# Kernel optimization log

Measured on AMD Instinct MI355X. Metric: run time of the kernel, lower is better.

## Reference

```python
import jax, jax.numpy as jnp
import numpy as np

B, S, E, H = 2, 2048, 1024, 16
D = E // H  # head dimension = 64


def setup_inputs() -> dict:
    key = jax.random.key(0)
    ks = jax.random.split(key, 12)
    scale_in = 1.0 / np.sqrt(E)
    x = jax.random.normal(ks[0], (B, S, E), dtype=jnp.float32)
    # random 0/1 attention mask (1 = attend, 0 = masked out)
    mask = jax.random.randint(ks[1], (B, S, S), 0, 2, dtype=jnp.int32)
    # per-head QKV projections, stacked over the head axis: [H, E, D]
    Wq = jax.random.normal(ks[2], (H, E, D), dtype=jnp.float32) * scale_in
    bq = jnp.zeros((H, D), dtype=jnp.float32)
    Wk = jax.random.normal(ks[3], (H, E, D), dtype=jnp.float32) * scale_in
    bk = jnp.zeros((H, D), dtype=jnp.float32)
    Wv = jax.random.normal(ks[4], (H, E, D), dtype=jnp.float32) * scale_in
    bv = jnp.zeros((H, D), dtype=jnp.float32)
    # output projection: [H*D, E] == [E, E]
    Wo = jax.random.normal(ks[5], (H * D, E), dtype=jnp.float32) * scale_in
    bo = jnp.zeros((E,), dtype=jnp.float32)
    return {"x": x, "mask": mask, "Wq": Wq, "bq": bq, "Wk": Wk, "bk": bk,
            "Wv": Wv, "bv": bv, "Wo": Wo, "bo": bo}


def reference(x, mask, Wq, bq, Wk, bk, Wv, bv, Wo, bo):
    # Batched equivalent of the per-head Python loop: all heads at once.
    q = jnp.einsum('bse,hed->bhsd', x, Wq) + bq[None, :, None, :]  # [B,H,S,D]
    k = jnp.einsum('bse,hed->bhsd', x, Wk) + bk[None, :, None, :]
    v = jnp.einsum('bse,hed->bhsd', x, Wv) + bv[None, :, None, :]
    scale = 1.0 / jnp.sqrt(jnp.asarray(D, dtype=q.dtype))
    scores = jnp.einsum('bhsd,bhtd->bhst', q, k) * scale          # [B,H,S,S]
    scores = jnp.where(mask[:, None, :, :] != 0, scores, jnp.asarray(-1e9, scores.dtype))
    attn = jax.nn.softmax(scores, axis=-1)
    ctx = jnp.einsum('bhst,bhtd->bhsd', attn, v)                  # [B,H,S,D]
    # concat heads along feature dim (torch.cat(dim=2))
    concat = jnp.transpose(ctx, (0, 2, 1, 3)).reshape(B, S, H * D)
    return concat @ Wo + bo
```

## Files before the change

kernel.cpp:

```cpp
#include <hip/hip_runtime.h>

#define S_LEN 2048
#define EMB   1024
#define NH    16
#define HD    64
#define BS    2

typedef __bf16 bf16;
typedef bf16  bf16x8 __attribute__((ext_vector_type(8)));
typedef bf16  bf16x4 __attribute__((ext_vector_type(4)));
typedef float f32x4  __attribute__((ext_vector_type(4)));
typedef unsigned long long u64;

__device__ __forceinline__ bf16x8 ld8(const bf16* p){ return *(const bf16x8*)p; }

#define SW(row, g) ((((g) ^ ((row) & 7))) * 8)

__global__ __launch_bounds__(256)
void pack_mask(const int* __restrict__ mask, u64* __restrict__ pm)
{
    int lane = threadIdx.x & 63;
    int row  = blockIdx.x * 4 + (threadIdx.x >> 6);
    const int* mr = mask + (size_t)row * S_LEN;
    u64* pr = pm + (size_t)row * (S_LEN / 64);
    for (int i = 0; i < S_LEN / 64; ++i) {
        u64 bits = __ballot(mr[i * 64 + lane] != 0);
        if (lane == 0) pr[i] = bits;
    }
}

__global__ __launch_bounds__(256)
void transpose_w(const float* __restrict__ W0, const float* __restrict__ W1,
                 const float* __restrict__ W2, const float* __restrict__ W3,
                 bf16* __restrict__ Wt)
{
    const int z = blockIdx.z;
    const float* W = z == 0 ? W0 : z == 1 ? W1 : z == 2 ? W2 : W3;
    const bool head = z < 3;
    const int k0 = blockIdx.x * 64, n0 = blockIdx.y * 64;
    const int tid = threadIdx.x;
    __shared__ float T[64][68];
    {
        int k = k0 + (tid >> 2), cg = (tid & 3) * 16;
        size_t base = head ? ((size_t)(n0 >> 6) * ((size_t)EMB * HD) + (size_t)k * HD + cg)
                           : ((size_t)k * EMB + n0 + cg);
        #pragma unroll
        for (int g = 0; g < 4; ++g) {
            f32x4 v = *(const f32x4*)(W + base + g * 4);
            #pragma unroll
            for (int j = 0; j < 4; ++j) T[tid >> 2][cg + g * 4 + j] = v[j];
        }
    }
    __syncthreads();
    {
        int n = n0 + (tid >> 2), ck = (tid & 3) * 16;
        bf16 t16[16];
        #pragma unroll
        for (int j = 0; j < 16; ++j) t16[j] = (bf16)T[ck + j][tid >> 2];
        bf16* outp = Wt + (size_t)z * EMB * EMB + (size_t)n * EMB + k0 + ck;
        *(bf16x8*)outp       = *(bf16x8*)t16;
        *(bf16x8*)(outp + 8) = *(bf16x8*)(t16 + 8);
    }
}

__global__ __launch_bounds__(256)
void cvt_f32_bf16(const float* __restrict__ x, bf16* __restrict__ y)
{
    size_t i = ((size_t)blockIdx.x * 256 + threadIdx.x) * 16;
    bf16 t[16];
    #pragma unroll
    for (int g = 0; g < 4; ++g) {
        f32x4 v = *(const f32x4*)(x + i + g * 4);
        #pragma unroll
        for (int j = 0; j < 4; ++j) t[g * 4 + j] = (bf16)v[j];
    }
    *(bf16x8*)(y + i)     = *(bf16x8*)t;
    *(bf16x8*)(y + i + 8) = *(bf16x8*)(t + 8);
}

__global__ __launch_bounds__(512)
void gemm128(const void* __restrict__ Ap, const float* __restrict__ Wp,
             const bf16* __restrict__ Wtp, const float* __restrict__ bias,
             void* __restrict__ Cp, int N, int K, int whead,
             int m_base, int a32, int cmode)
{
    const int tid  = threadIdx.x;
    const int lane = tid & 63, quad = lane >> 4, c = lane & 15;
    const int w = tid >> 6, wm = w >> 2, wn = w & 3;
    const int m0 = blockIdx.x * 128, n0 = blockIdx.y * 128;

    __shared__ bf16 Ash[128][64];
    __shared__ bf16 Wsh[128][64];

    f32x4 acc[4][2];
    #pragma unroll
    for (int mt = 0; mt < 4; ++mt)
        #pragma unroll
        for (int nt = 0; nt < 2; ++nt) acc[mt][nt] = (f32x4){0.f,0.f,0.f,0.f};

    const int arow = tid >> 2, aq = tid & 3;

    auto compute = [&]() {
        #pragma unroll
        for (int kh = 0; kh < 2; ++kh) {
            bf16x8 bfr[2];
            #pragma unroll
            for (int nt = 0; nt < 2; ++nt) {
                int rw = wn * 32 + nt * 16 + c;
                bfr[nt] = ld8(&Wsh[rw][SW(rw, kh * 4 + quad)]);
            }
            #pragma unroll
            for (int mt = 0; mt < 4; ++mt) {
                int ra = wm * 64 + mt * 16 + c;
                bf16x8 af = ld8(&Ash[ra][SW(ra, kh * 4 + quad)]);
                #pragma unroll
                for (int nt = 0; nt < 2; ++nt)
                    acc[mt][nt] = __builtin_amdgcn_mfma_f32_16x16x32_bf16(af, bfr[nt], acc[mt][nt], 0, 0, 0);
            }
        }
    };

    if (Wtp) {
        bf16x8 ar[2]; f32x4 a32r[4]; bf16x8 wr[2];
        auto loadT = [&](int k0) {
            if (a32) {
                const float* A = (const float*)Ap + (size_t)(m_base + m0 + arow) * K + k0 + aq * 16;
                #pragma unroll
                for (int g = 0; g < 4; ++g) a32r[g] = *(const f32x4*)(A + g * 4);
            } else {
                const bf16* A = (const bf16*)Ap + (size_t)(m_base + m0 + arow) * K + k0 + aq * 16;
                ar[0] = ld8(A); ar[1] = ld8(A + 8);
            }
            const bf16* Wr = Wtp + (size_t)(n0 + arow) * K + k0 + aq * 16;
            wr[0] = ld8(Wr); wr[1] = ld8(Wr + 8);
        };
        auto storeT = [&]() {
            bf16x8 av[2];
            if (a32) {
                bf16 t16[16];
                #pragma unroll
                for (int g = 0; g < 4; ++g)
                    #pragma unroll
                    for (int j = 0; j < 4; ++j) t16[g * 4 + j] = (bf16)a32r[g][j];
                av[0] = *(bf16x8*)t16; av[1] = *(bf16x8*)(t16 + 8);
            } else { av[0] = ar[0]; av[1] = ar[1]; }
            #pragma unroll
            for (int g2 = 0; g2 < 2; ++g2) {
                *(bf16x8*)&Ash[arow][SW(arow, aq * 2 + g2)] = av[g2];
                *(bf16x8*)&Wsh[arow][SW(arow, aq * 2 + g2)] = wr[g2];
            }
        };
        loadT(0);
        for (int k0 = 0; k0 < K; k0 += 64) {
            __syncthreads();
            storeT();
            __syncthreads();
            if (k0 + 64 < K) loadT(k0 + 64);
            compute();
        }
    } else {
        for (int k0 = 0; k0 < K; k0 += 64) {
            __syncthreads();
            if (a32) {
                const float* A = (const float*)Ap + (size_t)(m_base + m0 + arow) * K + k0 + aq * 16;
                bf16 t16[16];
                #pragma unroll
                for (int g = 0; g < 4; ++g) {
                    f32x4 v = *(const f32x4*)(A + g * 4);
                    #pragma unroll
                    for (int j = 0; j < 4; ++j) t16[g * 4 + j] = (bf16)v[j];
                }
                *(bf16x8*)&Ash[arow][SW(arow, aq * 2)]     = *(bf16x8*)t16;
                *(bf16x8*)&Ash[arow][SW(arow, aq * 2 + 1)] = *(bf16x8*)(t16 + 8);
            } else {
                const bf16* A = (const bf16*)Ap + (size_t)(m_base + m0 + arow) * K + k0 + aq * 16;
                *(bf16x8*)&Ash[arow][SW(arow, aq * 2)]     = ld8(A);
                *(bf16x8*)&Ash[arow][SW(arow, aq * 2 + 1)] = ld8(A + 8);
            }
            {
                int nl = tid & 127, kg = tid >> 7;
                int n = n0 + nl;
                size_t base    = whead ? ((size_t)(n >> 6) * ((size_t)K * HD) + (n & 63))
                                       : (size_t)n;
                size_t kstride = whead ? (size_t)HD : (size_t)N;
                #pragma unroll
                for (int p = 0; p < 2; ++p) {
                    int grp = kg + 4 * p;
                    bf16 t8[8];
                    #pragma unroll
                    for (int j = 0; j < 8; ++j)
                        t8[j] = (bf16)Wp[base + (size_t)(k0 + grp * 8 + j) * kstride];
                    *(bf16x8*)&Wsh[nl][SW(nl, grp)] = *(bf16x8*)t8;
                }
            }
            __syncthreads();
            compute();
        }
    }

    #pragma unroll
    for (int nt = 0; nt < 2; ++nt) {
        int n = n0 + wn * 32 + nt * 16 + c;
        float bv = bias[n];
        #pragma unroll
        for (int mt = 0; mt < 4; ++mt)
            #pragma unroll
            for (int r = 0; r < 4; ++r) {
                int m = m0 + wm * 64 + mt * 16 + quad * 4 + r;
                float v = acc[mt][nt][r] + bv;
                if (cmode == 0)      ((bf16*)Cp)[(size_t)m * N + n] = (bf16)v;
                else if (cmode == 1) ((float*)Cp)[(size_t)m * N + n] = v;
                else {
                    int mm = m_base + m;
                    ((bf16*)Cp)[((size_t)((mm >> 11) * NH + (n >> 6)) * HD + (n & 63)) * S_LEN + (mm & 2047)] = (bf16)v;
                }
            }
    }
}

__global__ __launch_bounds__(256)
void attn_kernel(bf16* q0p, bf16* q1p, const bf16* __restrict__ kbuf,
                 const bf16* __restrict__ VTg, const u64* __restrict__ pmask)
{
    const int tid  = threadIdx.x;
    const int w    = tid >> 6;
    const int lane = tid & 63;
    const int quad = lane >> 4;
    const int c    = lane & 15;
    const int q0   = blockIdx.x * 128;
    const int bh   = blockIdx.y;
    const int b    = bh >> 4, h = bh & 15;

    bf16* qc = b ? q1p : q0p;
    const bf16* kh_ = kbuf + (size_t)b * S_LEN * EMB + h * HD;
    const bf16* vt  = VTg + (size_t)bh * HD * S_LEN;

    __shared__ bf16 Ksh [64][64];
    __shared__ bf16 VTsh[64][64];
    __shared__ bf16 Psh[4][32][64];

    bf16x8 qf[2][2];
    #pragma unroll
    for (int st = 0; st < 2; ++st)
        #pragma unroll
        for (int kk = 0; kk < 2; ++kk)
            qf[st][kk] = ld8(qc + (size_t)(q0 + w * 32 + st * 16 + c) * EMB + h * HD + kk * 32 + quad * 8);

    const u64* pmr0 = pmask + (size_t)(b * S_LEN + q0 + w * 32 + c) * (S_LEN / 64);
    const u64* pmr1 = pmr0 + (size_t)16 * (S_LEN / 64);

    float l[2] = {0.f, 0.f};
    f32x4 o[2][4];
    #pragma unroll
    for (int st = 0; st < 2; ++st)
        #pragma unroll
        for (int dt = 0; dt < 4; ++dt) o[st][dt] = (f32x4){0.f,0.f,0.f,0.f};

    const int srow = tid >> 2, sg = (tid & 3) * 2;
    bf16x8 kr[2], vr[2];
    auto loadKV = [&](int t0) {
        const bf16* kp = kh_ + (size_t)(t0 + srow) * EMB + sg * 8;
        kr[0] = ld8(kp); kr[1] = ld8(kp + 8);
        const bf16* vp = vt + (size_t)srow * S_LEN + t0 + sg * 8;
        vr[0] = ld8(vp); vr[1] = ld8(vp + 8);
    };

    loadKV(0);
    for (int t0 = 0; t0 < S_LEN; t0 += 64) {
        __syncthreads();
        #pragma unroll
        for (int g2 = 0; g2 < 2; ++g2) {
            *(bf16x8*)&Ksh [srow][SW(srow, sg + g2)] = kr[g2];
            *(bf16x8*)&VTsh[srow][SW(srow, sg + g2)] = vr[g2];
        }
        __syncthreads();
        if (t0 + 64 < S_LEN) loadKV(t0 + 64);

        u64 pm0 = pmr0[t0 >> 6], pm1 = pmr1[t0 >> 6];

        f32x4 sc[2][4];
        #pragma unroll
        for (int st = 0; st < 2; ++st)
            #pragma unroll
            for (int tt = 0; tt < 4; ++tt) sc[st][tt] = (f32x4){0.f,0.f,0.f,0.f};
        #pragma unroll
        for (int tt = 0; tt < 4; ++tt)
            #pragma unroll
            for (int kk = 0; kk < 2; ++kk) {
                int rk = tt * 16 + c;
                bf16x8 ka = ld8(&Ksh[rk][SW(rk, kk * 4 + quad)]);
                sc[0][tt] = __builtin_amdgcn_mfma_f32_16x16x32_bf16(ka, qf[0][kk], sc[0][tt], 0, 0, 0);
                sc[1][tt] = __builtin_amdgcn_mfma_f32_16x16x32_bf16(ka, qf[1][kk], sc[1][tt], 0, 0, 0);
            }

        #pragma unroll
        for (int st = 0; st < 2; ++st) {
            u64 pm = st ? pm1 : pm0;
            int prow = st * 16 + c;
            #pragma unroll
            for (int tt = 0; tt < 4; ++tt) {
                bf16x4 pv;
                #pragma unroll
                for (int r = 0; r < 4; ++r) {
                    float e = __expf(sc[st][tt][r] * 0.125f);
                    e = ((pm >> (tt * 16 + quad * 4 + r)) & 1) ? e : 0.f;
                    l[st] += e;
                    pv[r] = (bf16)e;
                }
                *(bf16x4*)&Psh[w][prow][SW(prow, tt * 2 + (quad >> 1)) + (quad & 1) * 4] = pv;
            }
        }
        __builtin_amdgcn_s_waitcnt(0xc07f);

        #pragma unroll
        for (int th = 0; th < 2; ++th) {
            bf16x8 pf0 = ld8(&Psh[w][c]     [SW(c,      th * 4 + quad)]);
            bf16x8 pf1 = ld8(&Psh[w][16 + c][SW(16 + c, th * 4 + quad)]);
            #pragma unroll
            for (int dt = 0; dt < 4; ++dt) {
                int rv = dt * 16 + c;
                bf16x8 av = ld8(&VTsh[rv][SW(rv, th * 4 + quad)]);
                o[0][dt] = __builtin_amdgcn_mfma_f32_16x16x32_bf16(av, pf0, o[0][dt], 0, 0, 0);
                o[1][dt] = __builtin_amdgcn_mfma_f32_16x16x32_bf16(av, pf1, o[1][dt], 0, 0, 0);
            }
        }
    }

    #pragma unroll
    for (int st = 0; st < 2; ++st) {
        float ls = l[st];
        ls += __shfl_xor(ls, 16);
        ls += __shfl_xor(ls, 32);
        float inv = 1.0f / fmaxf(ls, 1e-30f);
        #pragma unroll
        for (int dt = 0; dt < 4; ++dt) {
            bf16x4 ov;
            #pragma unroll
            for (int r = 0; r < 4; ++r) ov[r] = (bf16)(o[st][dt][r] * inv);
            *(bf16x4*)&qc[(size_t)(q0 + w * 32 + st * 16 + c) * EMB + h * HD + dt * 16 + quad * 4] = ov;
        }
    }
}

extern "C" void kernel_launch(void* const* d_in, const int* in_sizes, int n_in,
                              void* d_out, int out_size, void* d_ws, size_t ws_size,
                              hipStream_t stream)
{
    const float* x    = (const float*)d_in[0];
    const int*   mask = (const int*)d_in[1];
    const float* Wq   = (const float*)d_in[2];
    const float* bq   = (const float*)d_in[3];
    const float* Wk   = (const float*)d_in[4];
    const float* bk   = (const float*)d_in[5];
    const float* Wv   = (const float*)d_in[6];
    const float* bv   = (const float*)d_in[7];
    const float* Wo   = (const float*)d_in[8];
    const float* bo   = (const float*)d_in[9];
    float* out = (float*)d_out;

    const size_t SLAB = (size_t)S_LEN * EMB;
    const size_t QB = (size_t)BS * SLAB * sizeof(bf16);
    const size_t WT = (size_t)4 * EMB * EMB * sizeof(bf16);
    const size_t PM = (size_t)BS * S_LEN * (S_LEN / 64) * 8;
    const size_t XB = (size_t)BS * SLAB * sizeof(bf16);

    bf16* VT = (bf16*)d_out;
    bf16* kb = (bf16*)d_out + BS * SLAB;

    dim3 b256(256), b512(512);
    dim3 gFull(BS * S_LEN / 128, EMB / 128);
    dim3 gHalf(S_LEN / 128, EMB / 128);
    dim3 gAtt (S_LEN / 128, BS * NH);
    dim3 gT   (EMB / 64, EMB / 64, 4);
    dim3 gPk  (BS * S_LEN / 4);

    if (ws_size >= QB + WT + PM + 64) {
        bf16* qb  = (bf16*)d_ws;
        bf16* Wt  = (bf16*)((char*)d_ws + QB);
        u64*  pm  = (u64*)((char*)d_ws + QB + WT);
        const void* xA = x; int a32 = 1;
        if (ws_size >= QB + WT + PM + XB + 64) {
            bf16* xbf = (bf16*)((char*)d_ws + QB + WT + PM);
            cvt_f32_bf16<<<dim3(1024), b256, 0, stream>>>(x, xbf);
            xA = xbf; a32 = 0;
        }
        pack_mask<<<gPk, b256, 0, stream>>>(mask, pm);
        transpose_w<<<gT, b256, 0, stream>>>(Wq, Wk, Wv, Wo, Wt);

        gemm128<<<gFull, b512, 0, stream>>>(xA, nullptr, Wt + 1 * EMB * EMB, bk, kb, EMB, EMB, 0, 0, a32, 0);
        gemm128<<<gFull, b512, 0, stream>>>(xA, nullptr, Wt + 2 * EMB * EMB, bv, VT, EMB, EMB, 0, 0, a32, 2);
        gemm128<<<gFull, b512, 0, stream>>>(xA, nullptr, Wt + 0 * EMB * EMB, bq, qb, EMB, EMB, 0, 0, a32, 0);

        attn_kernel<<<gAtt, b256, 0, stream>>>(qb, qb + SLAB, kb, VT, pm);

        gemm128<<<gFull, b512, 0, stream>>>(qb, nullptr, Wt + 3 * EMB * EMB, bo, out, EMB, EMB, 0, 0, 0, 1);
    } else if (ws_size >= QB + PM + 64) {
        bf16* qb = (bf16*)d_ws;
        u64*  pm = (u64*)((char*)d_ws + QB);
        pack_mask<<<gPk, b256, 0, stream>>>(mask, pm);

        gemm128<<<gFull, b512, 0, stream>>>(x, Wk, nullptr, bk, kb, EMB, EMB, 1, 0, 1, 0);
        gemm128<<<gFull, b512, 0, stream>>>(x, Wv, nullptr, bv, VT, EMB, EMB, 1, 0, 1, 2);
        gemm128<<<gFull, b512, 0, stream>>>(x, Wq, nullptr, bq, qb, EMB, EMB, 1, 0, 1, 0);

        attn_kernel<<<gAtt, b256, 0, stream>>>(qb, qb + SLAB, kb, VT, pm);

        gemm128<<<gFull, b512, 0, stream>>>(qb, Wo, nullptr, bo, out, EMB, EMB, 0, 0, 0, 1);
    } else {
        bf16* qb0 = (bf16*)d_in[4];
        bf16* qb1 = (bf16*)d_in[6];
        u64*  pm  = (u64*)d_in[2];

        gemm128<<<gFull, b512, 0, stream>>>(x, Wk, nullptr, bk, kb, EMB, EMB, 1, 0, 1, 0);
        gemm128<<<gFull, b512, 0, stream>>>(x, Wv, nullptr, bv, VT, EMB, EMB, 1, 0, 1, 2);
        gemm128<<<gHalf, b512, 0, stream>>>(x, Wq, nullptr, bq, qb0, EMB, EMB, 1, 0,     1, 0);
        gemm128<<<gHalf, b512, 0, stream>>>(x, Wq, nullptr, bq, qb1, EMB, EMB, 1, S_LEN, 1, 0);
        pack_mask<<<gPk, b256, 0, stream>>>(mask, pm);

        attn_kernel<<<gAtt, b256, 0, stream>>>(qb0, qb1, kb, VT, pm);

        gemm128<<<gHalf, b512, 0, stream>>>(qb0, Wo, nullptr, bo, out,        EMB, EMB, 0, 0, 0, 1);
        gemm128<<<gHalf, b512, 0, stream>>>(qb1, Wo, nullptr, bo, out + SLAB, EMB, EMB, 0, 0, 0, 1);
    }
}
```

Before: 288.5 us.

## Fuse QKV GEMMs, use direct global-to-LDS loads, fold softmax scale into Q

```diff
diff --git a/kernel.cpp b/kernel.cpp
--- a/kernel.cpp
+++ b/kernel.cpp
@@ -5,14 +5,23 @@
 #define NH    16
 #define HD    64
 #define BS    2
+#define QSCALE 0.18033688f
 
 typedef __bf16 bf16;
 typedef bf16  bf16x8 __attribute__((ext_vector_type(8)));
 typedef bf16  bf16x4 __attribute__((ext_vector_type(4)));
 typedef float f32x4  __attribute__((ext_vector_type(4)));
 typedef unsigned long long u64;
+typedef unsigned int u32;
 
 __device__ __forceinline__ bf16x8 ld8(const bf16* p){ return *(const bf16x8*)p; }
+
+__device__ __forceinline__ void gl_lds16(const bf16* g, void* l) {
+    __builtin_amdgcn_global_load_lds(
+        (const __attribute__((address_space(1))) void*)g,
+        (__attribute__((address_space(3))) void*)l,
+        16, 0, 0);
+}
 
 #define SW(row, g) ((((g) ^ ((row) & 7))) * 8)
 
@@ -78,6 +87,166 @@
     *(bf16x8*)(y + i + 8) = *(bf16x8*)(t + 8);
 }
 
+__global__ __launch_bounds__(256)
+void scale_q(bf16* __restrict__ q)
+{
+    size_t i = ((size_t)blockIdx.x * 256 + threadIdx.x) * 8;
+    bf16x8 v = *(bf16x8*)(q + i);
+    #pragma unroll
+    for (int j = 0; j < 8; ++j) v[j] = (bf16)((float)v[j] * QSCALE);
+    *(bf16x8*)(q + i) = v;
+}
+
+__global__ __launch_bounds__(256)
+void gemm_qkv(const void* __restrict__ Ap, const bf16* __restrict__ Wt,
+              const float* __restrict__ bqp, const float* __restrict__ bkp,
+              const float* __restrict__ bvp,
+              bf16* __restrict__ qb, bf16* __restrict__ kb, bf16* __restrict__ VT,
+              int a32)
+{
+    const int tid  = threadIdx.x;
+    const int lane = tid & 63, quad = lane >> 4, c = lane & 15;
+    const int w = tid >> 6, wm = w >> 1, wn = w & 1;
+    const int m0 = blockIdx.x * 128;
+    const int n0 = blockIdx.y * 128;
+
+    __shared__ bf16 Ash[128][64];
+    __shared__ bf16 Wsh[128][64];
+
+    f32x4 acc[4][4];
+    #pragma unroll
+    for (int mt = 0; mt < 4; ++mt)
+        #pragma unroll
+        for (int nt = 0; nt < 4; ++nt) acc[mt][nt] = (f32x4){0.f,0.f,0.f,0.f};
+
+    const int lrow = lane >> 3, lcol = (lane & 7) * 8;
+
+    for (int k0 = 0; k0 < EMB; k0 += 64) {
+        __syncthreads();
+        if (!a32) {
+            const bf16* A = (const bf16*)Ap;
+            #pragma unroll
+            for (int j = 0; j < 4; ++j)
+                gl_lds16(A + (size_t)(m0 + w * 32 + j * 8 + lrow) * EMB + k0 + lcol,
+                         &Ash[w * 32 + j * 8][0]);
+        } else {
+            const float* A = (const float*)Ap + (size_t)(m0 + (tid >> 1)) * EMB + k0 + (tid & 1) * 32;
+            bf16 t[32];
+            #pragma unroll
+            for (int g = 0; g < 8; ++g) {
+                f32x4 v = *(const f32x4*)(A + g * 4);
+                #pragma unroll
+                for (int j = 0; j < 4; ++j) t[g * 4 + j] = (bf16)v[j];
+            }
+            #pragma unroll
+            for (int g2 = 0; g2 < 4; ++g2)
+                *(bf16x8*)&Ash[tid >> 1][(tid & 1) * 32 + g2 * 8] = *(bf16x8*)(t + g2 * 8);
+        }
+        #pragma unroll
+        for (int j = 0; j < 4; ++j)
+            gl_lds16(Wt + (size_t)(n0 + w * 32 + j * 8 + lrow) * EMB + k0 + lcol,
+                     &Wsh[w * 32 + j * 8][0]);
+        __syncthreads();
+
+        #pragma unroll
+        for (int kh = 0; kh < 2; ++kh) {
+            bf16x8 af[4], bfv[4];
+            #pragma unroll
+            for (int mt = 0; mt < 4; ++mt) af[mt]  = ld8(&Ash[wm * 64 + mt * 16 + c][kh * 32 + quad * 8]);
+            #pragma unroll
+            for (int nt = 0; nt < 4; ++nt) bfv[nt] = ld8(&Wsh[wn * 64 + nt * 16 + c][kh * 32 + quad * 8]);
+            #pragma unroll
+            for (int mt = 0; mt < 4; ++mt)
+                #pragma unroll
+                for (int nt = 0; nt < 4; ++nt)
+                    acc[mt][nt] = __builtin_amdgcn_mfma_f32_16x16x32_bf16(af[mt], bfv[nt], acc[mt][nt], 0, 0, 0);
+        }
+    }
+
+    const int z = n0 >> 10;
+    const float* bias = z == 0 ? bqp : z == 1 ? bkp : bvp;
+    #pragma unroll
+    for (int nt = 0; nt < 4; ++nt) {
+        int nn = (n0 & 1023) + wn * 64 + nt * 16 + c;
+        float bv_ = bias[nn];
+        #pragma unroll
+        for (int mt = 0; mt < 4; ++mt)
+            #pragma unroll
+            for (int r = 0; r < 4; ++r) {
+                int m = m0 + wm * 64 + mt * 16 + quad * 4 + r;
+                float v = acc[mt][nt][r] + bv_;
+                if (z == 0)      qb[(size_t)m * EMB + nn] = (bf16)(v * QSCALE);
+                else if (z == 1) kb[(size_t)m * EMB + nn] = (bf16)v;
+                else {
+                    int head = nn >> 6, d = nn & 63;
+                    VT[((size_t)((m >> 11) * NH + head) * HD + d) * S_LEN + (m & 2047)] = (bf16)v;
+                }
+            }
+    }
+}
+
+__global__ __launch_bounds__(256)
+void gemm_o(const bf16* __restrict__ Ap, const bf16* __restrict__ Wt,
+            const float* __restrict__ bo, float* __restrict__ C)
+{
+    const int tid  = threadIdx.x;
+    const int lane = tid & 63, quad = lane >> 4, c = lane & 15;
+    const int w = tid >> 6, wm = w >> 1, wn = w & 1;
+    const int m0 = blockIdx.x * 128;
+    const int n0 = blockIdx.y * 64;
+
+    __shared__ bf16 Ash[128][64];
+    __shared__ bf16 Wsh[64][64];
+
+    f32x4 acc[4][2];
+    #pragma unroll
+    for (int mt = 0; mt < 4; ++mt)
+        #pragma unroll
+        for (int nt = 0; nt < 2; ++nt) acc[mt][nt] = (f32x4){0.f,0.f,0.f,0.f};
+
+    const int lrow = lane >> 3, lcol = (lane & 7) * 8;
+
+    for (int k0 = 0; k0 < EMB; k0 += 64) {
+        __syncthreads();
+        #pragma unroll
+        for (int j = 0; j < 4; ++j)
+            gl_lds16(Ap + (size_t)(m0 + w * 32 + j * 8 + lrow) * EMB + k0 + lcol,
+                     &Ash[w * 32 + j * 8][0]);
+        #pragma unroll
+        for (int j = 0; j < 2; ++j)
+            gl_lds16(Wt + (size_t)(n0 + w * 16 + j * 8 + lrow) * EMB + k0 + lcol,
+                     &Wsh[w * 16 + j * 8][0]);
+        __syncthreads();
+
+        #pragma unroll
+        for (int kh = 0; kh < 2; ++kh) {
+            bf16x8 af[4], bfv[2];
+            #pragma unroll
+            for (int mt = 0; mt < 4; ++mt) af[mt]  = ld8(&Ash[wm * 64 + mt * 16 + c][kh * 32 + quad * 8]);
+            #pragma unroll
+            for (int nt = 0; nt < 2; ++nt) bfv[nt] = ld8(&Wsh[wn * 32 + nt * 16 + c][kh * 32 + quad * 8]);
+            #pragma unroll
+            for (int mt = 0; mt < 4; ++mt)
+                #pragma unroll
+                for (int nt = 0; nt < 2; ++nt)
+                    acc[mt][nt] = __builtin_amdgcn_mfma_f32_16x16x32_bf16(af[mt], bfv[nt], acc[mt][nt], 0, 0, 0);
+        }
+    }
+
+    #pragma unroll
+    for (int nt = 0; nt < 2; ++nt) {
+        int n = n0 + wn * 32 + nt * 16 + c;
+        float bv_ = bo[n];
+        #pragma unroll
+        for (int mt = 0; mt < 4; ++mt)
+            #pragma unroll
+            for (int r = 0; r < 4; ++r) {
+                int m = m0 + wm * 64 + mt * 16 + quad * 4 + r;
+                C[(size_t)m * EMB + n] = acc[mt][nt][r] + bv_;
+            }
+    }
+}
+
 __global__ __launch_bounds__(512)
 void gemm128(const void* __restrict__ Ap, const float* __restrict__ Wp,
              const bf16* __restrict__ Wtp, const float* __restrict__ bias,
@@ -120,94 +289,54 @@
         }
     };
 
-    if (Wtp) {
-        bf16x8 ar[2]; f32x4 a32r[4]; bf16x8 wr[2];
-        auto loadT = [&](int k0) {
-            if (a32) {
-                const float* A = (const float*)Ap + (size_t)(m_base + m0 + arow) * K + k0 + aq * 16;
-                #pragma unroll
-                for (int g = 0; g < 4; ++g) a32r[g] = *(const f32x4*)(A + g * 4);
-            } else {
-                const bf16* A = (const bf16*)Ap + (size_t)(m_base + m0 + arow) * K + k0 + aq * 16;
-                ar[0] = ld8(A); ar[1] = ld8(A + 8);
-            }
-            const bf16* Wr = Wtp + (size_t)(n0 + arow) * K + k0 + aq * 16;
-            wr[0] = ld8(Wr); wr[1] = ld8(Wr + 8);
-        };
-        auto storeT = [&]() {
-            bf16x8 av[2];
-            if (a32) {
-                bf16 t16[16];
-                #pragma unroll
-                for (int g = 0; g < 4; ++g)
-                    #pragma unroll
-                    for (int j = 0; j < 4; ++j) t16[g * 4 + j] = (bf16)a32r[g][j];
-                av[0] = *(bf16x8*)t16; av[1] = *(bf16x8*)(t16 + 8);
-            } else { av[0] = ar[0]; av[1] = ar[1]; }
-            #pragma unroll
-            for (int g2 = 0; g2 < 2; ++g2) {
-                *(bf16x8*)&Ash[arow][SW(arow, aq * 2 + g2)] = av[g2];
-                *(bf16x8*)&Wsh[arow][SW(arow, aq * 2 + g2)] = wr[g2];
-            }
-        };
-        loadT(0);
-        for (int k0 = 0; k0 < K; k0 += 64) {
-            __syncthreads();
-            storeT();
-            __syncthreads();
-            if (k0 + 64 < K) loadT(k0 + 64);
-            compute();
-        }
-    } else {
-        for (int k0 = 0; k0 < K; k0 += 64) {
-            __syncthreads();
-            if (a32) {
-                const float* A = (const float*)Ap + (size_t)(m_base + m0 + arow) * K + k0 + aq * 16;
-                bf16 t16[16];
-                #pragma unroll
-                for (int g = 0; g < 4; ++g) {
-                    f32x4 v = *(const f32x4*)(A + g * 4);
-                    #pragma unroll
-                    for (int j = 0; j < 4; ++j) t16[g * 4 + j] = (bf16)v[j];
-                }
-                *(bf16x8*)&Ash[arow][SW(arow, aq * 2)]     = *(bf16x8*)t16;
-                *(bf16x8*)&Ash[arow][SW(arow, aq * 2 + 1)] = *(bf16x8*)(t16 + 8);
-            } else {
-                const bf16* A = (const bf16*)Ap + (size_t)(m_base + m0 + arow) * K + k0 + aq * 16;
-                *(bf16x8*)&Ash[arow][SW(arow, aq * 2)]     = ld8(A);
-                *(bf16x8*)&Ash[arow][SW(arow, aq * 2 + 1)] = ld8(A + 8);
-            }
-            {
-                int nl = tid & 127, kg = tid >> 7;
-                int n = n0 + nl;
-                size_t base    = whead ? ((size_t)(n >> 6) * ((size_t)K * HD) + (n & 63))
-                                       : (size_t)n;
-                size_t kstride = whead ? (size_t)HD : (size_t)N;
-                #pragma unroll
-                for (int p = 0; p < 2; ++p) {
-                    int grp = kg + 4 * p;
-                    bf16 t8[8];
-                    #pragma unroll
-                    for (int j = 0; j < 8; ++j)
-                        t8[j] = (bf16)Wp[base + (size_t)(k0 + grp * 8 + j) * kstride];
-                    *(bf16x8*)&Wsh[nl][SW(nl, grp)] = *(bf16x8*)t8;
-                }
-            }
-            __syncthreads();
-            compute();
-        }
+    for (int k0 = 0; k0 < K; k0 += 64) {
+        __syncthreads();
+        if (a32) {
+            const float* A = (const float*)Ap + (size_t)(m_base + m0 + arow) * K + k0 + aq * 16;
+            bf16 t16[16];
+            #pragma unroll
+            for (int g = 0; g < 4; ++g) {
+                f32x4 v = *(const f32x4*)(A + g * 4);
+                #pragma unroll
+                for (int j = 0; j < 4; ++j) t16[g * 4 + j] = (bf16)v[j];
+            }
+            *(bf16x8*)&Ash[arow][SW(arow, aq * 2)]     = *(bf16x8*)t16;
+            *(bf16x8*)&Ash[arow][SW(arow, aq * 2 + 1)] = *(bf16x8*)(t16 + 8);
+        } else {
+            const bf16* A = (const bf16*)Ap + (size_t)(m_base + m0 + arow) * K + k0 + aq * 16;
+            *(bf16x8*)&Ash[arow][SW(arow, aq * 2)]     = ld8(A);
+            *(bf16x8*)&Ash[arow][SW(arow, aq * 2 + 1)] = ld8(A + 8);
+        }
+        {
+            int nl = tid & 127, kg = tid >> 7;
+            int n = n0 + nl;
+            size_t base    = whead ? ((size_t)(n >> 6) * ((size_t)K * HD) + (n & 63))
+                                   : (size_t)n;
+            size_t kstride = whead ? (size_t)HD : (size_t)N;
+            #pragma unroll
+            for (int p = 0; p < 2; ++p) {
+                int grp = kg + 4 * p;
+                bf16 t8[8];
+                #pragma unroll
+                for (int j = 0; j < 8; ++j)
+                    t8[j] = (bf16)Wp[base + (size_t)(k0 + grp * 8 + j) * kstride];
+                *(bf16x8*)&Wsh[nl][SW(nl, grp)] = *(bf16x8*)t8;
+            }
+        }
+        __syncthreads();
+        compute();
     }
 
     #pragma unroll
     for (int nt = 0; nt < 2; ++nt) {
         int n = n0 + wn * 32 + nt * 16 + c;
-        float bv = bias[n];
+        float bv_ = bias[n];
         #pragma unroll
         for (int mt = 0; mt < 4; ++mt)
             #pragma unroll
             for (int r = 0; r < 4; ++r) {
                 int m = m0 + wm * 64 + mt * 16 + quad * 4 + r;
-                float v = acc[mt][nt][r] + bv;
+                float v = acc[mt][nt][r] + bv_;
                 if (cmode == 0)      ((bf16*)Cp)[(size_t)m * N + n] = (bf16)v;
                 else if (cmode == 1) ((float*)Cp)[(size_t)m * N + n] = v;
                 else {
@@ -249,7 +378,7 @@
     const u64* pmr0 = pmask + (size_t)(b * S_LEN + q0 + w * 32 + c) * (S_LEN / 64);
     const u64* pmr1 = pmr0 + (size_t)16 * (S_LEN / 64);
 
-    float l[2] = {0.f, 0.f};
+    f32x4 l4[2] = {(f32x4){0.f,0.f,0.f,0.f}, (f32x4){0.f,0.f,0.f,0.f}};
     f32x4 o[2][4];
     #pragma unroll
     for (int st = 0; st < 2; ++st)
@@ -276,7 +405,9 @@
         __syncthreads();
         if (t0 + 64 < S_LEN) loadKV(t0 + 64);
 
-        u64 pm0 = pmr0[t0 >> 6], pm1 = pmr1[t0 >> 6];
+        u64 s0 = pmr0[t0 >> 6] >> (quad * 4);
+        u64 s1 = pmr1[t0 >> 6] >> (quad * 4);
+        u32 mm[2][2] = {{(u32)s0, (u32)(s0 >> 32)}, {(u32)s1, (u32)(s1 >> 32)}};
 
         f32x4 sc[2][4];
         #pragma unroll
@@ -295,16 +426,16 @@
 
         #pragma unroll
         for (int st = 0; st < 2; ++st) {
-            u64 pm = st ? pm1 : pm0;
             int prow = st * 16 + c;
             #pragma unroll
             for (int tt = 0; tt < 4; ++tt) {
+                u32 half = mm[st][tt >> 1];
                 bf16x4 pv;
                 #pragma unroll
                 for (int r = 0; r < 4; ++r) {
-                    float e = __expf(sc[st][tt][r] * 0.125f);
-                    e = ((pm >> (tt * 16 + quad * 4 + r)) & 1) ? e : 0.f;
-                    l[st] += e;
+                    float e = __builtin_amdgcn_exp2f(sc[st][tt][r]);
+                    e = ((half >> ((tt & 1) * 16 + r)) & 1) ? e : 0.f;
+                    l4[st][r] += e;
                     pv[r] = (bf16)e;
                 }
                 *(bf16x4*)&Psh[w][prow][SW(prow, tt * 2 + (quad >> 1)) + (quad & 1) * 4] = pv;
@@ -328,7 +459,7 @@
 
     #pragma unroll
     for (int st = 0; st < 2; ++st) {
-        float ls = l[st];
+        float ls = l4[st][0] + l4[st][1] + l4[st][2] + l4[st][3];
         ls += __shfl_xor(ls, 16);
         ls += __shfl_xor(ls, 32);
         float inv = 1.0f / fmaxf(ls, 1e-30f);
@@ -368,11 +499,11 @@
     bf16* kb = (bf16*)d_out + BS * SLAB;
 
     dim3 b256(256), b512(512);
-    dim3 gFull(BS * S_LEN / 128, EMB / 128);
-    dim3 gHalf(S_LEN / 128, EMB / 128);
     dim3 gAtt (S_LEN / 128, BS * NH);
     dim3 gT   (EMB / 64, EMB / 64, 4);
     dim3 gPk  (BS * S_LEN / 4);
+    dim3 gFull(BS * S_LEN / 128, EMB / 128);
+    dim3 gHalf(S_LEN / 128, EMB / 128);
 
     if (ws_size >= QB + WT + PM + 64) {
         bf16* qb  = (bf16*)d_ws;
@@ -387,13 +518,13 @@
         pack_mask<<<gPk, b256, 0, stream>>>(mask, pm);
         transpose_w<<<gT, b256, 0, stream>>>(Wq, Wk, Wv, Wo, Wt);
 
-        gemm128<<<gFull, b512, 0, stream>>>(xA, nullptr, Wt + 1 * EMB * EMB, bk, kb, EMB, EMB, 0, 0, a32, 0);
-        gemm128<<<gFull, b512, 0, stream>>>(xA, nullptr, Wt + 2 * EMB * EMB, bv, VT, EMB, EMB, 0, 0, a32, 2);
-        gemm128<<<gFull, b512, 0, stream>>>(xA, nullptr, Wt + 0 * EMB * EMB, bq, qb, EMB, EMB, 0, 0, a32, 0);
+        gemm_qkv<<<dim3(BS * S_LEN / 128, 3 * EMB / 128), b256, 0, stream>>>(
+            xA, Wt, bq, bk, bv, qb, kb, VT, a32);
 
         attn_kernel<<<gAtt, b256, 0, stream>>>(qb, qb + SLAB, kb, VT, pm);
 
-        gemm128<<<gFull, b512, 0, stream>>>(qb, nullptr, Wt + 3 * EMB * EMB, bo, out, EMB, EMB, 0, 0, 0, 1);
+        gemm_o<<<dim3(BS * S_LEN / 128, EMB / 64), b256, 0, stream>>>(
+            qb, Wt + (size_t)3 * EMB * EMB, bo, out);
     } else if (ws_size >= QB + PM + 64) {
         bf16* qb = (bf16*)d_ws;
         u64*  pm = (u64*)((char*)d_ws + QB);
@@ -402,6 +533,7 @@
         gemm128<<<gFull, b512, 0, stream>>>(x, Wk, nullptr, bk, kb, EMB, EMB, 1, 0, 1, 0);
         gemm128<<<gFull, b512, 0, stream>>>(x, Wv, nullptr, bv, VT, EMB, EMB, 1, 0, 1, 2);
         gemm128<<<gFull, b512, 0, stream>>>(x, Wq, nullptr, bq, qb, EMB, EMB, 1, 0, 1, 0);
+        scale_q<<<dim3(BS * SLAB / (256 * 8)), b256, 0, stream>>>(qb);
 
         attn_kernel<<<gAtt, b256, 0, stream>>>(qb, qb + SLAB, kb, VT, pm);
 
@@ -415,6 +547,8 @@
         gemm128<<<gFull, b512, 0, stream>>>(x, Wv, nullptr, bv, VT, EMB, EMB, 1, 0, 1, 2);
         gemm128<<<gHalf, b512, 0, stream>>>(x, Wq, nullptr, bq, qb0, EMB, EMB, 1, 0,     1, 0);
         gemm128<<<gHalf, b512, 0, stream>>>(x, Wq, nullptr, bq, qb1, EMB, EMB, 1, S_LEN, 1, 0);
+        scale_q<<<dim3(SLAB / (256 * 8)), b256, 0, stream>>>(qb0);
+        scale_q<<<dim3(SLAB / (256 * 8)), b256, 0, stream>>>(qb1);
         pack_mask<<<gPk, b256, 0, stream>>>(mask, pm);
 
         attn_kernel<<<gAtt, b256, 0, stream>>>(qb0, qb1, kb, VT, pm);
```

Result: faster. 260.4 us (-9.8%).
